# Optimization experiments

Hardware: AMD Instinct MI355X
Metric: run time of the kernel (lower is better)

## Reference

```python
import jax, jax.numpy as jnp
import numpy as np

T, B, E, H = 2048, 64, 512, 512
SIGMA = 0.01

def setup_inputs() -> dict:
    key = jax.random.key(0)
    kx, kwxh, kwhh = jax.random.split(key, 3)
    X = jax.random.normal(kx, (T, B, E), dtype=jnp.float32)
    W_xh = jax.random.normal(kwxh, (E, H), dtype=jnp.float32) * SIGMA
    W_hh = jax.random.normal(kwhh, (H, H), dtype=jnp.float32) * SIGMA
    b_h = jnp.zeros((H,), dtype=jnp.float32)
    return {"X": X, "W_xh": W_xh, "W_hh": W_hh, "b_h": b_h}

def reference(X, W_xh, W_hh, b_h):
    # Precompute input projection for all timesteps in one big GEMM:
    # [T, B, E] @ [E, H] -> [T, B, H]
    Xp = jnp.einsum('tbe,eh->tbh', X, W_xh) + b_h
    h0 = jnp.zeros((X.shape[1], W_hh.shape[0]), dtype=X.dtype)

    def step(h, xp_t):
        h_new = jnp.tanh(xp_t + h @ W_hh)
        return h_new, h_new

    h_last, hidden_states = jax.lax.scan(step, h0, Xp)
    return hidden_states, h_last
```

## Files before the change

kernel.cpp:

```cpp
#include <hip/hip_runtime.h>


typedef short bf16x8 __attribute__((ext_vector_type(8)));
typedef float f32x4 __attribute__((ext_vector_type(4)));

#define T_STEPS 2048
#define BATCH 64
#define HDIM 512
#define EDIM 512
#define BH (BATCH * HDIM)
#define NWG2 16
#define HA_STRIDE 520
#define STG_STRIDE 36

__device__ __forceinline__ short f2bf(float x) {
  unsigned u = __float_as_uint(x);
  u = (u + 0x7FFFu + ((u >> 16) & 1u)) >> 16;
  return (short)u;
}

__global__ __launch_bounds__(256) void xp_gemm(const float* __restrict__ X,
                                               const float* __restrict__ Wxh,
                                               const float* __restrict__ bh,
                                               float* __restrict__ out) {
  __shared__ short As[64][40];
  __shared__ short Bs[64][40];
  const int bid = blockIdx.x;
  const int xcd = bid & 7;
  const int s   = bid >> 3;
  const int mt  = (xcd << 8) + (s >> 3);
  const int nt  = s & 7;
  const int tid = threadIdx.x;
  const int lane = tid & 63;
  const int wv   = tid >> 6;
  const int mrow = (wv >> 1) * 32;
  const int ncol = (wv & 1) * 32;

  f32x4 acc00 = {0.f,0.f,0.f,0.f};
  f32x4 acc01 = acc00, acc10 = acc00, acc11 = acc00;

  const int ar = tid >> 2, aq = tid & 3;
  const int bk = tid >> 3, bn = (tid & 7) * 8;

  for (int kt = 0; kt < 16; ++kt) {
    const float* asrc = X + (size_t)(mt * 64 + ar) * EDIM + kt * 32 + aq * 8;
    f32x4 a0 = *(const f32x4*)asrc;
    f32x4 a1 = *(const f32x4*)(asrc + 4);
    const float* bsrc = Wxh + (size_t)(kt * 32 + bk) * HDIM + nt * 64 + bn;
    f32x4 w0 = *(const f32x4*)bsrc;
    f32x4 w1 = *(const f32x4*)(bsrc + 4);

    bf16x8 ap;
    ap[0] = f2bf(a0[0]); ap[1] = f2bf(a0[1]); ap[2] = f2bf(a0[2]); ap[3] = f2bf(a0[3]);
    ap[4] = f2bf(a1[0]); ap[5] = f2bf(a1[1]); ap[6] = f2bf(a1[2]); ap[7] = f2bf(a1[3]);
    *(bf16x8*)&As[ar][aq * 8] = ap;
    Bs[bn + 0][bk] = f2bf(w0[0]);
    Bs[bn + 1][bk] = f2bf(w0[1]);
    Bs[bn + 2][bk] = f2bf(w0[2]);
    Bs[bn + 3][bk] = f2bf(w0[3]);
    Bs[bn + 4][bk] = f2bf(w1[0]);
    Bs[bn + 5][bk] = f2bf(w1[1]);
    Bs[bn + 6][bk] = f2bf(w1[2]);
    Bs[bn + 7][bk] = f2bf(w1[3]);
    __syncthreads();

    const int fm = lane & 15, fq = (lane >> 4) * 8;
    bf16x8 fa0 = *(bf16x8*)&As[mrow + fm][fq];
    bf16x8 fa1 = *(bf16x8*)&As[mrow + 16 + fm][fq];
    bf16x8 fb0 = *(bf16x8*)&Bs[ncol + fm][fq];
    bf16x8 fb1 = *(bf16x8*)&Bs[ncol + 16 + fm][fq];
    acc00 = __builtin_amdgcn_mfma_f32_16x16x32_bf16(fa0, fb0, acc00, 0, 0, 0);
    acc01 = __builtin_amdgcn_mfma_f32_16x16x32_bf16(fa0, fb1, acc01, 0, 0, 0);
    acc10 = __builtin_amdgcn_mfma_f32_16x16x32_bf16(fa1, fb0, acc10, 0, 0, 0);
    acc11 = __builtin_amdgcn_mfma_f32_16x16x32_bf16(fa1, fb1, acc11, 0, 0, 0);
    __syncthreads();
  }

  const int c = lane & 15, r4 = (lane >> 4) * 4;
  #pragma unroll
  for (int i = 0; i < 4; ++i) {
    int gm0 = mt * 64 + mrow + r4 + i;
    int gm1 = gm0 + 16;
    int gn0 = nt * 64 + ncol + c;
    int gn1 = gn0 + 16;
    out[(size_t)gm0 * HDIM + gn0] = acc00[i] + bh[gn0];
    out[(size_t)gm0 * HDIM + gn1] = acc01[i] + bh[gn1];
    out[(size_t)gm1 * HDIM + gn0] = acc10[i] + bh[gn0];
    out[(size_t)gm1 * HDIM + gn1] = acc11[i] + bh[gn1];
  }
}

__global__ __launch_bounds__(256, 1) void rnn_scan2(const float* __restrict__ Whh,
                                                    float* __restrict__ out,
                                                    int* __restrict__ flags,
                                                    short* __restrict__ slot0,
                                                    short* __restrict__ slot1) {
  __shared__ short hA[64 * HA_STRIDE];
  __shared__ float stg[64][STG_STRIDE];

  const int tid  = threadIdx.x;
  const int g    = blockIdx.x;
  const int n0   = g * 32;
  const int w    = tid >> 6;
  const int lane = tid & 63;
  const int ln   = lane & 15;
  const int kq   = (lane >> 4) * 8;
  const int r0   = (lane >> 4) * 4;
  const int mbase = w * 16;

  bf16x8 Bf[2][16];
  #pragma unroll
  for (int nt = 0; nt < 2; ++nt) {
    #pragma unroll
    for (int ks = 0; ks < 16; ++ks) {
      const float* src = Whh + (size_t)(ks * 32 + kq) * HDIM + n0 + nt * 16 + ln;
      bf16x8 f;
      #pragma unroll
      for (int j = 0; j < 8; ++j) f[j] = f2bf(src[(size_t)j * HDIM]);
      Bf[nt][ks] = f;
    }
  }

  for (int i = tid; i < 64 * HA_STRIDE; i += 256) hA[i] = 0;
  __syncthreads();

  const int b  = tid >> 2;
  const int c0 = (tid & 3) * 8;

  for (int t = 0; t < T_STEPS; ++t) {
    const size_t xbase = (size_t)t * BH + (size_t)(mbase + r0) * HDIM + n0 + ln;
    f32x4 acc0, acc1;
    #pragma unroll
    for (int i = 0; i < 4; ++i) {
      acc0[i] = out[xbase + (size_t)i * HDIM];
      acc1[i] = out[xbase + (size_t)i * HDIM + 16];
    }

    if (t > 0) {
      if (tid < NWG2) {
        const int slot = (t - 1) * NWG2 + tid;
        while (__hip_atomic_load(&flags[slot], __ATOMIC_RELAXED,
                                 __HIP_MEMORY_SCOPE_AGENT) == 0)
          __builtin_amdgcn_s_sleep(2);
      }
      __syncthreads();
      __threadfence();
      const short* sprev = ((t - 1) & 1) ? slot1 : slot0;
      #pragma unroll
      for (int i = 0; i < 16; ++i) {
        const int r = mbase + i;
        const short* gp = sprev + (size_t)r * HDIM + lane * 8;
        __builtin_amdgcn_global_load_lds(
            (const __attribute__((address_space(1))) void*)gp,
            (__attribute__((address_space(3))) void*)&hA[r * HA_STRIDE],
            16, 0, 0);
      }
    }
    __syncthreads();

    const short* arow = &hA[(mbase + ln) * HA_STRIDE + kq];
    #pragma unroll
    for (int ks = 0; ks < 16; ++ks) {
      bf16x8 a = *(const bf16x8*)(arow + ks * 32);
      acc0 = __builtin_amdgcn_mfma_f32_16x16x32_bf16(a, Bf[0][ks], acc0, 0, 0, 0);
      acc1 = __builtin_amdgcn_mfma_f32_16x16x32_bf16(a, Bf[1][ks], acc1, 0, 0, 0);
    }

    #pragma unroll
    for (int i = 0; i < 4; ++i) {
      stg[mbase + r0 + i][ln]      = tanhf(acc0[i]);
      stg[mbase + r0 + i][ln + 16] = tanhf(acc1[i]);
    }
    __syncthreads();

    {
      f32x4 lo = *(const f32x4*)&stg[b][c0];
      f32x4 hi = *(const f32x4*)&stg[b][c0 + 4];
      float* op = out + (size_t)t * BH + (size_t)b * HDIM + n0 + c0;
      *(f32x4*)op = lo;
      *(f32x4*)(op + 4) = hi;
      short* scur = (((t & 1) ? slot1 : slot0) + (size_t)b * HDIM + n0 + c0);
      bf16x8 pk;
      pk[0] = f2bf(lo[0]); pk[1] = f2bf(lo[1]); pk[2] = f2bf(lo[2]); pk[3] = f2bf(lo[3]);
      pk[4] = f2bf(hi[0]); pk[5] = f2bf(hi[1]); pk[6] = f2bf(hi[2]); pk[7] = f2bf(hi[3]);
      *(bf16x8*)scur = pk;
      if (t == T_STEPS - 1) {
        float* lp = out + (size_t)T_STEPS * BH + (size_t)b * HDIM + n0 + c0;
        *(f32x4*)lp = lo;
        *(f32x4*)(lp + 4) = hi;
      }
    }

    __threadfence();
    __syncthreads();
    if (tid == 0)
      __hip_atomic_store(&flags[t * NWG2 + g], 1,
                         __ATOMIC_RELEASE, __HIP_MEMORY_SCOPE_AGENT);
  }
}

extern "C" void kernel_launch(void* const* d_in, const int* in_sizes, int n_in,
                              void* d_out, int out_size, void* d_ws, size_t ws_size,
                              hipStream_t stream) {
  const float* X   = (const float*)d_in[0];
  const float* Wxh = (const float*)d_in[1];
  const float* Whh = (const float*)d_in[2];
  const float* bh  = (const float*)d_in[3];
  float* out = (float*)d_out;

  int*   flags = (int*)d_ws;
  short* slot0 = (short*)((char*)d_ws + (size_t)T_STEPS * NWG2 * sizeof(int));
  short* slot1 = slot0 + (size_t)BATCH * HDIM;

  hipMemsetAsync(d_ws, 0, (size_t)T_STEPS * NWG2 * sizeof(int), stream);
  xp_gemm<<<dim3(16384), dim3(256), 0, stream>>>(X, Wxh, bh, out);
  rnn_scan2<<<dim3(NWG2), dim3(256), 0, stream>>>(Whh, out, flags, slot0, slot1);
}
```

Measured before the change: 12.75 ms.

## Split batch across independent workgroups to remove inter-block flag synchronization

The recurrent scan is repartitioned so each of 4 workgroups owns 16 batch rows and the full hidden width. Batch rows are independent, so the per-step global flag polling, the fences and the global hidden-state exchange all go away, leaving only block-local barriers. W_hh is split across register fragments, an LDS copy, and per-step L2 reloads of a repacked bf16 copy produced by a new small kernel. A fast exp/reciprocal tanh replaces tanhf. The trade-off is fewer active CUs and more weight traffic per step.

```diff
diff --git a/kernel.cpp b/kernel.cpp
--- a/kernel.cpp
+++ b/kernel.cpp
@@ -2,6 +2,7 @@
 
 
 typedef short bf16x8 __attribute__((ext_vector_type(8)));
+typedef short bf16x4 __attribute__((ext_vector_type(4)));
 typedef float f32x4 __attribute__((ext_vector_type(4)));
 
 #define T_STEPS 2048
@@ -9,14 +10,19 @@
 #define HDIM 512
 #define EDIM 512
 #define BH (BATCH * HDIM)
-#define NWG2 16
-#define HA_STRIDE 520
-#define STG_STRIDE 36
+#define NWG 4
+#define BPG 16
+#define HA_PITCH 520
 
 __device__ __forceinline__ short f2bf(float x) {
   unsigned u = __float_as_uint(x);
   u = (u + 0x7FFFu + ((u >> 16) & 1u)) >> 16;
   return (short)u;
+}
+
+__device__ __forceinline__ float fast_tanh(float x) {
+  float e = __expf(2.0f * x);
+  return 1.0f - 2.0f * __builtin_amdgcn_rcpf(e + 1.0f);
 }
 
 __global__ __launch_bounds__(256) void xp_gemm(const float* __restrict__ X,
@@ -90,112 +96,166 @@
   }
 }
 
-__global__ __launch_bounds__(256, 1) void rnn_scan2(const float* __restrict__ Whh,
+__global__ __launch_bounds__(64) void w_repack(const float* __restrict__ Whh,
+                                               short* __restrict__ wsW) {
+  const int blk = blockIdx.x;
+  const int w   = blk >> 3;
+  const int kk  = blk & 7;
+  const int lane = threadIdx.x;
+  const int ln = lane & 15;
+  const int kq = (lane >> 4) * 8;
+  const int ks = kk + 8;
+  #pragma unroll
+  for (int nt = 0; nt < 8; ++nt) {
+    const int col = w * 128 + nt * 16 + ln;
+    const float* src = Whh + (size_t)(ks * 32 + kq) * HDIM + col;
+    bf16x8 f;
+    #pragma unroll
+    for (int j = 0; j < 8; ++j) f[j] = f2bf(src[(size_t)j * HDIM]);
+    const int F = (w * 8 + kk) * 8 + nt;
+    *(bf16x8*)(wsW + (size_t)F * 512 + lane * 8) = f;
+  }
+}
+
+__global__ __launch_bounds__(256, 1) void rnn_scan3(const float* __restrict__ Whh,
                                                     float* __restrict__ out,
-                                                    int* __restrict__ flags,
-                                                    short* __restrict__ slot0,
-                                                    short* __restrict__ slot1) {
-  __shared__ short hA[64 * HA_STRIDE];
-  __shared__ float stg[64][STG_STRIDE];
+                                                    const short* __restrict__ wsW) {
+  __shared__ short WL[4 * 4 * 8 * 512];
+  __shared__ short hA[BPG * HA_PITCH];
 
   const int tid  = threadIdx.x;
   const int g    = blockIdx.x;
-  const int n0   = g * 32;
   const int w    = tid >> 6;
   const int lane = tid & 63;
   const int ln   = lane & 15;
   const int kq   = (lane >> 4) * 8;
   const int r0   = (lane >> 4) * 4;
-  const int mbase = w * 16;
-
-  bf16x8 Bf[2][16];
-  #pragma unroll
-  for (int nt = 0; nt < 2; ++nt) {
-    #pragma unroll
-    for (int ks = 0; ks < 16; ++ks) {
-      const float* src = Whh + (size_t)(ks * 32 + kq) * HDIM + n0 + nt * 16 + ln;
+
+  bf16x8 Wr[8][8];
+  #pragma unroll
+  for (int ks = 0; ks < 8; ++ks) {
+    #pragma unroll
+    for (int nt = 0; nt < 8; ++nt) {
+      const float* src = Whh + (size_t)(ks * 32 + kq) * HDIM + w * 128 + nt * 16 + ln;
       bf16x8 f;
       #pragma unroll
       for (int j = 0; j < 8; ++j) f[j] = f2bf(src[(size_t)j * HDIM]);
-      Bf[nt][ks] = f;
-    }
-  }
-
-  for (int i = tid; i < 64 * HA_STRIDE; i += 256) hA[i] = 0;
+      Wr[ks][nt] = f;
+    }
+  }
+
+  #pragma unroll
+  for (int kk = 0; kk < 4; ++kk) {
+    #pragma unroll
+    for (int nt = 0; nt < 8; ++nt) {
+      const short* gp = wsW + (size_t)((w * 8 + kk) * 8 + nt) * 512 + lane * 8;
+      __builtin_amdgcn_global_load_lds(
+          (const __attribute__((address_space(1))) void*)gp,
+          (__attribute__((address_space(3))) void*)&WL[((w * 4 + kk) * 8 + nt) * 512],
+          16, 0, 0);
+    }
+  }
+
+  for (int i = tid; i < BPG * HA_PITCH; i += 256) hA[i] = 0;
   __syncthreads();
 
-  const int b  = tid >> 2;
-  const int c0 = (tid & 3) * 8;
-
+  const size_t xrow = (size_t)(g * BPG + ln) * HDIM + w * 128 + r0;
+  const short* hbase = &hA[ln * HA_PITCH + kq];
+  const short* sbase = wsW + (size_t)w * 32768 + lane * 8;
+
+  #pragma unroll 1
   for (int t = 0; t < T_STEPS; ++t) {
-    const size_t xbase = (size_t)t * BH + (size_t)(mbase + r0) * HDIM + n0 + ln;
-    f32x4 acc0, acc1;
-    #pragma unroll
-    for (int i = 0; i < 4; ++i) {
-      acc0[i] = out[xbase + (size_t)i * HDIM];
-      acc1[i] = out[xbase + (size_t)i * HDIM + 16];
-    }
-
-    if (t > 0) {
-      if (tid < NWG2) {
-        const int slot = (t - 1) * NWG2 + tid;
-        while (__hip_atomic_load(&flags[slot], __ATOMIC_RELAXED,
-                                 __HIP_MEMORY_SCOPE_AGENT) == 0)
-          __builtin_amdgcn_s_sleep(2);
+    bf16x8 sA[8], sB[8];
+    #pragma unroll
+    for (int nt = 0; nt < 8; ++nt)
+      sA[nt] = *(const bf16x8*)(sbase + (size_t)(4 * 8 + nt) * 512);
+    #pragma unroll
+    for (int nt = 0; nt < 8; ++nt)
+      sB[nt] = *(const bf16x8*)(sbase + (size_t)(5 * 8 + nt) * 512);
+
+    f32x4 xp[8];
+    const float* xb = out + (size_t)t * BH + xrow;
+    #pragma unroll
+    for (int nt = 0; nt < 8; ++nt) xp[nt] = *(const f32x4*)(xb + nt * 16);
+
+    f32x4 acc[8];
+    #pragma unroll
+    for (int nt = 0; nt < 8; ++nt) acc[nt] = (f32x4){0.f, 0.f, 0.f, 0.f};
+
+    #pragma unroll
+    for (int ks = 0; ks < 4; ++ks) {
+      bf16x8 hf = *(const bf16x8*)(hbase + ks * 32);
+      #pragma unroll
+      for (int nt = 0; nt < 8; ++nt)
+        acc[nt] = __builtin_amdgcn_mfma_f32_16x16x32_bf16(Wr[ks][nt], hf, acc[nt], 0, 0, 0);
+    }
+    {
+      bf16x8 hf = *(const bf16x8*)(hbase + 12 * 32);
+      #pragma unroll
+      for (int nt = 0; nt < 8; ++nt)
+        acc[nt] = __builtin_amdgcn_mfma_f32_16x16x32_bf16(sA[nt], hf, acc[nt], 0, 0, 0);
+    }
+    #pragma unroll
+    for (int nt = 0; nt < 8; ++nt)
+      sA[nt] = *(const bf16x8*)(sbase + (size_t)(6 * 8 + nt) * 512);
+    #pragma unroll
+    for (int ks = 4; ks < 8; ++ks) {
+      bf16x8 hf = *(const bf16x8*)(hbase + ks * 32);
+      #pragma unroll
+      for (int nt = 0; nt < 8; ++nt)
+        acc[nt] = __builtin_amdgcn_mfma_f32_16x16x32_bf16(Wr[ks][nt], hf, acc[nt], 0, 0, 0);
+    }
+    {
+      bf16x8 hf = *(const bf16x8*)(hbase + 13 * 32);
+      #pragma unroll
+      for (int nt = 0; nt < 8; ++nt)
+        acc[nt] = __builtin_amdgcn_mfma_f32_16x16x32_bf16(sB[nt], hf, acc[nt], 0, 0, 0);
+    }
+    #pragma unroll
+    for (int nt = 0; nt < 8; ++nt)
+      sB[nt] = *(const bf16x8*)(sbase + (size_t)(7 * 8 + nt) * 512);
+    #pragma unroll
+    for (int kk = 0; kk < 4; ++kk) {
+      bf16x8 hf = *(const bf16x8*)(hbase + (8 + kk) * 32);
+      #pragma unroll
+      for (int nt = 0; nt < 8; ++nt) {
+        bf16x8 wl = *(const bf16x8*)&WL[((w * 4 + kk) * 8 + nt) * 512 + lane * 8];
+        acc[nt] = __builtin_amdgcn_mfma_f32_16x16x32_bf16(wl, hf, acc[nt], 0, 0, 0);
       }
-      __syncthreads();
-      __threadfence();
-      const short* sprev = ((t - 1) & 1) ? slot1 : slot0;
-      #pragma unroll
-      for (int i = 0; i < 16; ++i) {
-        const int r = mbase + i;
-        const short* gp = sprev + (size_t)r * HDIM + lane * 8;
-        __builtin_amdgcn_global_load_lds(
-            (const __attribute__((address_space(1))) void*)gp,
-            (__attribute__((address_space(3))) void*)&hA[r * HA_STRIDE],
-            16, 0, 0);
-      }
-    }
-    __syncthreads();
-
-    const short* arow = &hA[(mbase + ln) * HA_STRIDE + kq];
-    #pragma unroll
-    for (int ks = 0; ks < 16; ++ks) {
-      bf16x8 a = *(const bf16x8*)(arow + ks * 32);
-      acc0 = __builtin_amdgcn_mfma_f32_16x16x32_bf16(a, Bf[0][ks], acc0, 0, 0, 0);
-      acc1 = __builtin_amdgcn_mfma_f32_16x16x32_bf16(a, Bf[1][ks], acc1, 0, 0, 0);
-    }
-
-    #pragma unroll
-    for (int i = 0; i < 4; ++i) {
-      stg[mbase + r0 + i][ln]      = tanhf(acc0[i]);
-      stg[mbase + r0 + i][ln + 16] = tanhf(acc1[i]);
-    }
-    __syncthreads();
-
-    {
-      f32x4 lo = *(const f32x4*)&stg[b][c0];
-      f32x4 hi = *(const f32x4*)&stg[b][c0 + 4];
-      float* op = out + (size_t)t * BH + (size_t)b * HDIM + n0 + c0;
-      *(f32x4*)op = lo;
-      *(f32x4*)(op + 4) = hi;
-      short* scur = (((t & 1) ? slot1 : slot0) + (size_t)b * HDIM + n0 + c0);
-      bf16x8 pk;
-      pk[0] = f2bf(lo[0]); pk[1] = f2bf(lo[1]); pk[2] = f2bf(lo[2]); pk[3] = f2bf(lo[3]);
-      pk[4] = f2bf(hi[0]); pk[5] = f2bf(hi[1]); pk[6] = f2bf(hi[2]); pk[7] = f2bf(hi[3]);
-      *(bf16x8*)scur = pk;
-      if (t == T_STEPS - 1) {
-        float* lp = out + (size_t)T_STEPS * BH + (size_t)b * HDIM + n0 + c0;
-        *(f32x4*)lp = lo;
-        *(f32x4*)(lp + 4) = hi;
-      }
-    }
-
-    __threadfence();
-    __syncthreads();
-    if (tid == 0)
-      __hip_atomic_store(&flags[t * NWG2 + g], 1,
-                         __ATOMIC_RELEASE, __HIP_MEMORY_SCOPE_AGENT);
+    }
+    {
+      bf16x8 hf = *(const bf16x8*)(hbase + 14 * 32);
+      #pragma unroll
+      for (int nt = 0; nt < 8; ++nt)
+        acc[nt] = __builtin_amdgcn_mfma_f32_16x16x32_bf16(sA[nt], hf, acc[nt], 0, 0, 0);
+    }
+    {
+      bf16x8 hf = *(const bf16x8*)(hbase + 15 * 32);
+      #pragma unroll
+      for (int nt = 0; nt < 8; ++nt)
+        acc[nt] = __builtin_amdgcn_mfma_f32_16x16x32_bf16(sB[nt], hf, acc[nt], 0, 0, 0);
+    }
+
+    bf16x4 hp[8];
+    float* ob = out + (size_t)t * BH + xrow;
+    #pragma unroll
+    for (int nt = 0; nt < 8; ++nt) {
+      f32x4 v;
+      #pragma unroll
+      for (int i = 0; i < 4; ++i) v[i] = fast_tanh(acc[nt][i] + xp[nt][i]);
+      *(f32x4*)(ob + nt * 16) = v;
+      if (t == T_STEPS - 1)
+        *(f32x4*)(out + (size_t)T_STEPS * BH + xrow + nt * 16) = v;
+      bf16x4 p;
+      p[0] = f2bf(v[0]); p[1] = f2bf(v[1]); p[2] = f2bf(v[2]); p[3] = f2bf(v[3]);
+      hp[nt] = p;
+    }
+
+    __syncthreads();
+    #pragma unroll
+    for (int nt = 0; nt < 8; ++nt)
+      *(bf16x4*)&hA[ln * HA_PITCH + w * 128 + nt * 16 + r0] = hp[nt];
+    __syncthreads();
   }
 }
 
@@ -207,12 +267,9 @@
   const float* Whh = (const float*)d_in[2];
   const float* bh  = (const float*)d_in[3];
   float* out = (float*)d_out;
-
-  int*   flags = (int*)d_ws;
-  short* slot0 = (short*)((char*)d_ws + (size_t)T_STEPS * NWG2 * sizeof(int));
-  short* slot1 = slot0 + (size_t)BATCH * HDIM;
-
-  hipMemsetAsync(d_ws, 0, (size_t)T_STEPS * NWG2 * sizeof(int), stream);
+  short* wsW = (short*)d_ws;
+
+  w_repack<<<dim3(32), dim3(64), 0, stream>>>(Whh, wsW);
   xp_gemm<<<dim3(16384), dim3(256), 0, stream>>>(X, Wxh, bh, out);
-  rnn_scan2<<<dim3(NWG2), dim3(256), 0, stream>>>(Whh, out, flags, slot0, slot1);
-}
+  rnn_scan3<<<dim3(NWG), dim3(256), 0, stream>>>(Whh, out, wsW);
+}
```

Measured after the change: 11.20 ms. 12.2% less time.
